# Kernel tuning notes

Measured on AMD Instinct MI355X. Metric: run time of the kernel, lower is better.

The kernel has to match this reference:

```python
import jax, jax.numpy as jnp
import numpy as np

N = 100000
E = 1600000
IN_C = 64
HID = 32
HEADS = 4
OUT_C = 1
NEG_SLOPE = 0.2
BN_EPS = 1e-5


def setup_inputs() -> dict:
    key = jax.random.key(0)
    ks = jax.random.split(key, 12)
    x = jax.random.normal(ks[0], (N, IN_C), dtype=jnp.float32)
    edge_index = jax.random.randint(ks[1], (2, E), 0, N, dtype=jnp.int32)
    # GATConv layer 1: in -> heads*hid, concat=True
    W1 = jax.random.normal(ks[2], (IN_C, HEADS * HID), dtype=jnp.float32) * (1.0 / np.sqrt(IN_C))
    att_src1 = jax.random.normal(ks[3], (HEADS, HID), dtype=jnp.float32) * 0.1
    att_dst1 = jax.random.normal(ks[4], (HEADS, HID), dtype=jnp.float32) * 0.1
    b1 = jnp.zeros((HEADS * HID,), dtype=jnp.float32)
    # GATConv layer 2: heads*hid -> out, heads=1, concat=False
    W2 = jax.random.normal(ks[5], (HEADS * HID, OUT_C), dtype=jnp.float32) * (1.0 / np.sqrt(HEADS * HID))
    att_src2 = jax.random.normal(ks[6], (1, OUT_C), dtype=jnp.float32) * 0.1
    att_dst2 = jax.random.normal(ks[7], (1, OUT_C), dtype=jnp.float32) * 0.1
    b2 = jnp.zeros((OUT_C,), dtype=jnp.float32)
    # BatchNorm1d (eval mode, running stats)
    bn_gamma = jnp.ones((HEADS * HID,), dtype=jnp.float32)
    bn_beta = jnp.zeros((HEADS * HID,), dtype=jnp.float32)
    bn_mean = jnp.zeros((HEADS * HID,), dtype=jnp.float32)
    bn_var = jnp.ones((HEADS * HID,), dtype=jnp.float32)
    return {"x": x, "edge_index": edge_index, "W1": W1, "att_src1": att_src1,
            "att_dst1": att_dst1, "b1": b1, "W2": W2, "att_src2": att_src2,
            "att_dst2": att_dst2, "b2": b2, "bn_gamma": bn_gamma, "bn_beta": bn_beta,
            "bn_mean": bn_mean, "bn_var": bn_var}


def _gat_layer(x, src, dst, W, a_src, a_dst, heads, out_c, n):
    # linear transform, split heads: [N, heads, out_c]
    h = (x @ W).reshape(n, heads, out_c)
    # per-node attention terms: [N, heads]
    alpha_s = jnp.einsum('nhc,hc->nh', h, a_src)
    alpha_d = jnp.einsum('nhc,hc->nh', h, a_dst)
    # edge logits: [E, heads]
    e = jax.nn.leaky_relu(alpha_s[src] + alpha_d[dst], NEG_SLOPE)
    # segment softmax over edges sharing a destination node
    e_max = jax.ops.segment_max(e, dst, num_segments=n)
    e = jnp.exp(e - e_max[dst])
    denom = jax.ops.segment_sum(e, dst, num_segments=n)
    alpha = e / (denom[dst] + 1e-16)                 # [E, heads]
    msg = h[src] * alpha[:, :, None]                 # [E, heads, out_c]
    return jax.ops.segment_sum(msg, dst, num_segments=n)  # [N, heads, out_c]


def reference(x, edge_index, W1, att_src1, att_dst1, b1, W2, att_src2, att_dst2,
              b2, bn_gamma, bn_beta, bn_mean, bn_var):
    n = x.shape[0]
    loops = jnp.arange(n, dtype=edge_index.dtype)
    src = jnp.concatenate([edge_index[0], loops])    # PyG GATConv adds self-loops
    dst = jnp.concatenate([edge_index[1], loops])
    # layer 1: concat heads
    h = _gat_layer(x, src, dst, W1, att_src1, att_dst1, HEADS, HID, n)
    h = h.reshape(n, HEADS * HID) + b1
    # BatchNorm1d (eval) + ELU (dropout is identity in eval)
    h = (h - bn_mean) * jax.lax.rsqrt(bn_var + BN_EPS) * bn_gamma + bn_beta
    h = jax.nn.elu(h)
    # layer 2: single head, concat=False (mean over 1 head == squeeze)
    out = _gat_layer(h, src, dst, W2, att_src2, att_dst2, 1, OUT_C, n)
    return out.reshape(n, OUT_C) + b2
```

## Files before the change

### kernel.cpp

```cpp
#include <hip/hip_runtime.h>
#include <cstdint>
#include <cstddef>

#define NEG_SLOPE 0.2f
#define BN_EPS 1e-5f
#define BK_SHIFT 8
#define MAXBK 512
#define CHUNK 8192
#define CAP 8192

typedef _Float16 half4 __attribute__((ext_vector_type(4)));

__global__ void prep_kernel(const float* __restrict__ b1,
                            const float* __restrict__ bn_gamma,
                            const float* __restrict__ bn_beta,
                            const float* __restrict__ bn_mean,
                            const float* __restrict__ bn_var,
                            float* __restrict__ pre0,
                            float* __restrict__ pre1,
                            int* __restrict__ bucket_cursor) {
    int t = threadIdx.x;
    if (t < 128) {
        float sc = rsqrtf(bn_var[t] + BN_EPS) * bn_gamma[t];
        pre0[t] = sc;
        pre1[t] = (b1[t] - bn_mean[t]) * sc + bn_beta[t];
    }
    if (t < MAXBK) bucket_cursor[t] = 0;
}

__global__ void bin_kernel(const int* __restrict__ ei, int E, int N, int NBK,
                           int* __restrict__ bucket_cursor,
                           unsigned int* __restrict__ binned) {
    __shared__ int cnt[MAXBK];
    __shared__ int gstart[MAXBK];
    __shared__ int cur[MAXBK];
    int T = E + N;
    int tid = threadIdx.x;
    for (int b = tid; b < NBK; b += 256) { cnt[b] = 0; cur[b] = 0; }
    __syncthreads();
    int base = blockIdx.x * CHUNK;
    bool fast = (base + CHUNK <= E);
    if (fast) {
        for (int k = 0; k < CHUNK; k += 1024) {
            int i0 = base + k + tid;
            int d0 = ei[E + i0];
            int d1 = ei[E + i0 + 256];
            int d2 = ei[E + i0 + 512];
            int d3 = ei[E + i0 + 768];
            atomicAdd(&cnt[d0 >> BK_SHIFT], 1);
            atomicAdd(&cnt[d1 >> BK_SHIFT], 1);
            atomicAdd(&cnt[d2 >> BK_SHIFT], 1);
            atomicAdd(&cnt[d3 >> BK_SHIFT], 1);
        }
    } else {
        for (int k = 0; k < CHUNK; k += 256) {
            int i = base + k + tid;
            if (i < T) {
                int dst = (i < E) ? ei[E + i] : (i - E);
                atomicAdd(&cnt[dst >> BK_SHIFT], 1);
            }
        }
    }
    __syncthreads();
    for (int b = tid; b < NBK; b += 256) {
        int c = cnt[b];
        if (c) gstart[b] = atomicAdd(&bucket_cursor[b], c);
    }
    __syncthreads();
    if (fast) {
        for (int k = 0; k < CHUNK; k += 1024) {
            int i0 = base + k + tid;
            int s0 = ei[i0];
            int s1 = ei[i0 + 256];
            int s2 = ei[i0 + 512];
            int s3 = ei[i0 + 768];
            int d0 = ei[E + i0];
            int d1 = ei[E + i0 + 256];
            int d2 = ei[E + i0 + 512];
            int d3 = ei[E + i0 + 768];
            int b0 = d0 >> BK_SHIFT, b1 = d1 >> BK_SHIFT;
            int b2 = d2 >> BK_SHIFT, b3 = d3 >> BK_SHIFT;
            int p0 = gstart[b0] + atomicAdd(&cur[b0], 1);
            int p1 = gstart[b1] + atomicAdd(&cur[b1], 1);
            int p2 = gstart[b2] + atomicAdd(&cur[b2], 1);
            int p3 = gstart[b3] + atomicAdd(&cur[b3], 1);
            if (p0 < CAP) binned[(size_t)b0 * CAP + p0] =
                (unsigned int)s0 | ((unsigned int)(d0 & 255) << 24);
            if (p1 < CAP) binned[(size_t)b1 * CAP + p1] =
                (unsigned int)s1 | ((unsigned int)(d1 & 255) << 24);
            if (p2 < CAP) binned[(size_t)b2 * CAP + p2] =
                (unsigned int)s2 | ((unsigned int)(d2 & 255) << 24);
            if (p3 < CAP) binned[(size_t)b3 * CAP + p3] =
                (unsigned int)s3 | ((unsigned int)(d3 & 255) << 24);
        }
    } else {
        for (int k = 0; k < CHUNK; k += 256) {
            int i = base + k + tid;
            if (i < T) {
                int src, dst;
                if (i < E) { src = ei[i]; dst = ei[E + i]; }
                else       { src = i - E; dst = src; }
                int b = dst >> BK_SHIFT;
                int lp = gstart[b] + atomicAdd(&cur[b], 1);
                if (lp < CAP)
                    binned[(size_t)b * CAP + lp] =
                        (unsigned int)src | ((unsigned int)(dst & 255) << 24);
            }
        }
    }
}

__global__ void gemm_kernel(const float* __restrict__ x,
                            const float* __restrict__ W1,
                            const float* __restrict__ att_s,
                            const float* __restrict__ att_d,
                            _Float16* __restrict__ h0,
                            float* __restrict__ as1,
                            float* __restrict__ ad1,
                            int N) {
    __shared__ float xs[512];
    int tid = threadIdx.x;
    int n0b = blockIdx.x * 8;
    if (n0b >= N) return;
    {
        const float* __restrict__ xb = x + (size_t)n0b * 64;
        int lim = N - n0b; if (lim > 8) lim = 8;
        int nf = lim * 64;
        for (int i = tid; i < 512; i += 256)
            xs[i] = (i < nf) ? xb[i] : 0.f;
    }
    __syncthreads();
    int c = tid & 127;
    int pair = __builtin_amdgcn_readfirstlane(tid >> 7);
    int n0 = n0b + pair * 4;
    if (n0 >= N) return;
    float acc[4] = {0.f, 0.f, 0.f, 0.f};
    const float4* __restrict__ xq = (const float4*)&xs[pair * 256];
#pragma unroll 2
    for (int kk = 0; kk < 16; ++kk) {
        float4 x0 = xq[kk];
        float4 x1 = xq[16 + kk];
        float4 x2 = xq[32 + kk];
        float4 x3 = xq[48 + kk];
        const float* __restrict__ wp = &W1[kk * 4 * 128 + c];
        float w0 = wp[0];
        float w1 = wp[128];
        float w2 = wp[256];
        float w3 = wp[384];
        acc[0] = fmaf(x0.x, w0, acc[0]); acc[0] = fmaf(x0.y, w1, acc[0]);
        acc[0] = fmaf(x0.z, w2, acc[0]); acc[0] = fmaf(x0.w, w3, acc[0]);
        acc[1] = fmaf(x1.x, w0, acc[1]); acc[1] = fmaf(x1.y, w1, acc[1]);
        acc[1] = fmaf(x1.z, w2, acc[1]); acc[1] = fmaf(x1.w, w3, acc[1]);
        acc[2] = fmaf(x2.x, w0, acc[2]); acc[2] = fmaf(x2.y, w1, acc[2]);
        acc[2] = fmaf(x2.z, w2, acc[2]); acc[2] = fmaf(x2.w, w3, acc[2]);
        acc[3] = fmaf(x3.x, w0, acc[3]); acc[3] = fmaf(x3.y, w1, acc[3]);
        acc[3] = fmaf(x3.z, w2, acc[3]); acc[3] = fmaf(x3.w, w3, acc[3]);
    }
    float asc = att_s[c], adc = att_d[c];
    int head = c >> 5;
    int nn = N - n0; if (nn > 4) nn = 4;
#pragma unroll
    for (int i = 0; i < 4; ++i) {
        if (i >= nn) break;
        int n = n0 + i;
        h0[(size_t)n * 128 + c] = (_Float16)acc[i];
        float s = acc[i] * asc;
        float d = acc[i] * adc;
#pragma unroll
        for (int off = 16; off >= 1; off >>= 1) {
            s += __shfl_xor(s, off);
            d += __shfl_xor(d, off);
        }
        if ((threadIdx.x & 31) == 0) {
            as1[(size_t)n * 4 + head] = s;
            ad1[(size_t)n * 4 + head] = d;
        }
    }
}

__global__ void csr_kernel(const unsigned int* __restrict__ binned,
                           const int* __restrict__ bucket_cursor,
                           int N,
                           int* __restrict__ row_beg,
                           int* __restrict__ row_end,
                           int* __restrict__ csr_src) {
    __shared__ int cnt[256];
    __shared__ int cur[256];
    __shared__ int wsum[4];
    int b = blockIdx.x;
    int tid = threadIdx.x;
    int n0 = b << BK_SHIFT;
    int nr = N - n0; if (nr > 256) nr = 256;
    int tot = bucket_cursor[b];
    if (tot > CAP) tot = CAP;
    size_t base = (size_t)b * CAP;
    if (tid < 256) cnt[tid] = 0;
    __syncthreads();
    for (int j = tid; j < tot; j += 1024) {
        atomicAdd(&cnt[binned[base + j] >> 24], 1);
    }
    __syncthreads();
    int v = 0, incl = 0;
    int lane = tid & 63;
    int w = tid >> 6;
    if (tid < 256) {
        v = cnt[tid];
        incl = v;
#pragma unroll
        for (int off = 1; off < 64; off <<= 1) {
            int t = __shfl_up(incl, off);
            if (lane >= off) incl += t;
        }
        if (lane == 63) wsum[w] = incl;
    }
    __syncthreads();
    if (tid < 256) {
        int prefix = 0;
#pragma unroll
        for (int i = 0; i < 3; ++i)
            if (i < w) prefix += wsum[i];
        incl += prefix;
        int excl = incl - v;
        cur[tid] = excl;
        if (tid < nr) {
            row_beg[n0 + tid] = (int)base + excl;
            row_end[n0 + tid] = (int)base + incl;
        }
    }
    __syncthreads();
    for (int j = tid; j < tot; j += 1024) {
        unsigned int wv = binned[base + j];
        int pos = atomicAdd(&cur[wv >> 24], 1);
        csr_src[base + pos] = (int)(wv & 0xFFFFFFu);
    }
}

__global__ void gather1_kernel(const int* __restrict__ row_beg,
                               const int* __restrict__ row_end,
                               const int* __restrict__ csr_src,
                               const half4* __restrict__ h0,
                               const float* __restrict__ as1,
                               const float* __restrict__ ad1,
                               const float* __restrict__ pre0,
                               const float* __restrict__ pre1,
                               const float* __restrict__ W2,
                               float* __restrict__ h2, int N) {
    int n = blockIdx.x * 4 + (threadIdx.x >> 6);
    if (n >= N) return;
    int lane = threadIdx.x & 63;
    int sub  = lane & 31;
    int grp  = lane >> 5;
    int head = sub >> 3;
    float ad = ad1[((unsigned)n << 2) + head];
    int beg = row_beg[n];
    int end = row_end[n];
    float4 acc = make_float4(0.f, 0.f, 0.f, 0.f);
    float den = 0.f;
#pragma unroll 2
    for (int j = beg + grp; j < end; j += 2) {
        int src = csr_src[j];
        float as = as1[((unsigned)src << 2) + head];
        float lg = as + ad;
        float l = fmaf(NEG_SLOPE, fminf(lg, 0.f), fmaxf(lg, 0.f));
        float w = __expf(l);
        half4 hv = h0[((unsigned)src << 5) + sub];
        acc.x = fmaf(w, (float)hv.x, acc.x);
        acc.y = fmaf(w, (float)hv.y, acc.y);
        acc.z = fmaf(w, (float)hv.z, acc.z);
        acc.w = fmaf(w, (float)hv.w, acc.w);
        den += w;
    }
    acc.x += __shfl_xor(acc.x, 32);
    acc.y += __shfl_xor(acc.y, 32);
    acc.z += __shfl_xor(acc.z, 32);
    acc.w += __shfl_xor(acc.w, 32);
    den   += __shfl_xor(den, 32);
    float inv = 1.f / (den + 1e-16f);
    int c = sub * 4;
    float v0 = fmaf(acc.x * inv, pre0[c],     pre1[c]);
    float v1 = fmaf(acc.y * inv, pre0[c + 1], pre1[c + 1]);
    float v2 = fmaf(acc.z * inv, pre0[c + 2], pre1[c + 2]);
    float v3 = fmaf(acc.w * inv, pre0[c + 3], pre1[c + 3]);
    v0 = v0 > 0.f ? v0 : __expf(v0) - 1.f;
    v1 = v1 > 0.f ? v1 : __expf(v1) - 1.f;
    v2 = v2 > 0.f ? v2 : __expf(v2) - 1.f;
    v3 = v3 > 0.f ? v3 : __expf(v3) - 1.f;
    float t = v0 * W2[c] + v1 * W2[c + 1] + v2 * W2[c + 2] + v3 * W2[c + 3];
#pragma unroll
    for (int off = 16; off >= 1; off >>= 1) t += __shfl_xor(t, off);
    if (lane == 0) h2[n] = t;
}

__global__ void gather2_kernel(const int* __restrict__ row_beg,
                               const int* __restrict__ row_end,
                               const int* __restrict__ csr_src,
                               const float* __restrict__ h2,
                               const float* __restrict__ att_s2,
                               const float* __restrict__ att_d2,
                               const float* __restrict__ b2,
                               float* __restrict__ out, int N) {
    int n = blockIdx.x * 16 + (threadIdx.x >> 4);
    if (n >= N) return;
    int lane = threadIdx.x & 15;
    int beg = row_beg[n];
    int end = row_end[n];
    float a_s = att_s2[0];
    float a_d = att_d2[0];
    float hd = h2[n];
    float num = 0.f, den = 0.f;
    for (int j = beg + lane; j < end; j += 16) {
        int src = csr_src[j];
        float hs = h2[src];
        float lg = hs * a_s + hd * a_d;
        float l = fmaf(NEG_SLOPE, fminf(lg, 0.f), fmaxf(lg, 0.f));
        float w = __expf(l);
        num += w * hs;
        den += w;
    }
#pragma unroll
    for (int off = 8; off >= 1; off >>= 1) {
        num += __shfl_xor(num, off);
        den += __shfl_xor(den, off);
    }
    if (lane == 0) out[n] = num / (den + 1e-16f) + b2[0];
}

extern "C" void kernel_launch(void* const* d_in, const int* in_sizes, int n_in,
                              void* d_out, int out_size, void* d_ws, size_t ws_size,
                              hipStream_t stream) {
    const float* x     = (const float*)d_in[0];
    const int*   ei    = (const int*)  d_in[1];
    const float* W1    = (const float*)d_in[2];
    const float* atts1 = (const float*)d_in[3];
    const float* attd1 = (const float*)d_in[4];
    const float* b1    = (const float*)d_in[5];
    const float* W2    = (const float*)d_in[6];
    const float* atts2 = (const float*)d_in[7];
    const float* attd2 = (const float*)d_in[8];
    const float* b2    = (const float*)d_in[9];
    const float* bn_g  = (const float*)d_in[10];
    const float* bn_b  = (const float*)d_in[11];
    const float* bn_m  = (const float*)d_in[12];
    const float* bn_v  = (const float*)d_in[13];

    const int N = in_sizes[0] / 64;
    const int E = in_sizes[1] / 2;
    const int T = E + N;
    const int NBK = (N + 255) >> BK_SHIFT;
    const int NCH = (T + CHUNK - 1) / CHUNK;
    const int NGB = (N + 7) / 8;

    char* p = (char*)d_ws;
    auto alloc = [&](size_t bytes, size_t align) -> void* {
        uintptr_t q = ((uintptr_t)p + align - 1) & ~(uintptr_t)(align - 1);
        p = (char*)(q + bytes);
        return (void*)q;
    };
    _Float16* h0      = (_Float16*)alloc((size_t)N * 128 * 2, 16);
    float* as1        = (float*)alloc((size_t)N * 4 * 4, 16);
    float* ad1        = (float*)alloc((size_t)N * 4 * 4, 16);
    float* h2         = (float*)alloc((size_t)N * 4, 16);
    float* pre0       = (float*)alloc(128 * 4, 16);
    float* pre1       = (float*)alloc(128 * 4, 16);
    int*   row_beg    = (int*)alloc((size_t)N * 4, 16);
    int*   row_end    = (int*)alloc((size_t)N * 4, 16);
    int*   bucket_cur = (int*)alloc((size_t)MAXBK * 4, 16);
    unsigned int* binned = (unsigned int*)alloc((size_t)NBK * CAP * 4, 16);
    int*   csr_src    = (int*)alloc((size_t)NBK * CAP * 4, 16);

    prep_kernel<<<1, 512, 0, stream>>>(b1, bn_g, bn_b, bn_m, bn_v,
                                       pre0, pre1, bucket_cur);

    bin_kernel<<<NCH, 256, 0, stream>>>(ei, E, N, NBK, bucket_cur, binned);

    gemm_kernel<<<NGB, 256, 0, stream>>>(x, W1, atts1, attd1, h0, as1, ad1, N);

    csr_kernel<<<NBK, 1024, 0, stream>>>(binned, bucket_cur, N,
                                         row_beg, row_end, csr_src);

    gather1_kernel<<<(N + 3) / 4, 256, 0, stream>>>(
        row_beg, row_end, csr_src, (const half4*)h0, as1, ad1, pre0, pre1,
        W2, h2, N);

    gather2_kernel<<<(N + 15) / 16, 256, 0, stream>>>(
        row_beg, row_end, csr_src, h2, atts2, attd2, b2, (float*)d_out, N);
}
```

Measured before the change: 268.8 us.

## Merge bin and GEMM kernels into one launch; compute two columns per lane

The edge-binning kernel and the layer-1 GEMM kernel are combined into one launch, with the first NCH blocks doing binning and the rest doing the GEMM. This removes a launch and lets the two independent stages overlap on the device. The GEMM part is also restructured so each lane computes two adjacent output columns for 16 nodes per block, using paired weight loads and half2 stores. This cuts the number of GEMM blocks and the shuffle depth. In exchange, every block reserves the larger shared-memory footprint of both paths, which may reduce occupancy.

After: 261.2 us. -2.8%, faster.

```diff
diff --git a/kernel.cpp b/kernel.cpp
--- a/kernel.cpp
+++ b/kernel.cpp
@@ -10,6 +10,14 @@
 #define CAP 8192
 
 typedef _Float16 half4 __attribute__((ext_vector_type(4)));
+typedef _Float16 half2v __attribute__((ext_vector_type(2)));
+typedef float float2v __attribute__((ext_vector_type(2)));
+
+static __device__ __forceinline__ float2v fma2(float2v w, float s, float2v a) {
+    a.x = fmaf(s, w.x, a.x);
+    a.y = fmaf(s, w.y, a.y);
+    return a;
+}
 
 __global__ void prep_kernel(const float* __restrict__ b1,
                             const float* __restrict__ bn_gamma,
@@ -28,154 +36,165 @@
     if (t < MAXBK) bucket_cursor[t] = 0;
 }
 
-__global__ void bin_kernel(const int* __restrict__ ei, int E, int N, int NBK,
-                           int* __restrict__ bucket_cursor,
-                           unsigned int* __restrict__ binned) {
+__global__ void gemm_bin_kernel(
+                                const float* __restrict__ x,
+                                const float* __restrict__ W1,
+                                const float* __restrict__ att_s,
+                                const float* __restrict__ att_d,
+                                _Float16* __restrict__ h0,
+                                float* __restrict__ as1,
+                                float* __restrict__ ad1,
+                                int N,
+                                const int* __restrict__ ei, int E, int NBK,
+                                int* __restrict__ bucket_cursor,
+                                unsigned int* __restrict__ binned,
+                                int NCH) {
     __shared__ int cnt[MAXBK];
     __shared__ int gstart[MAXBK];
     __shared__ int cur[MAXBK];
-    int T = E + N;
-    int tid = threadIdx.x;
-    for (int b = tid; b < NBK; b += 256) { cnt[b] = 0; cur[b] = 0; }
-    __syncthreads();
-    int base = blockIdx.x * CHUNK;
-    bool fast = (base + CHUNK <= E);
-    if (fast) {
-        for (int k = 0; k < CHUNK; k += 1024) {
-            int i0 = base + k + tid;
-            int d0 = ei[E + i0];
-            int d1 = ei[E + i0 + 256];
-            int d2 = ei[E + i0 + 512];
-            int d3 = ei[E + i0 + 768];
-            atomicAdd(&cnt[d0 >> BK_SHIFT], 1);
-            atomicAdd(&cnt[d1 >> BK_SHIFT], 1);
-            atomicAdd(&cnt[d2 >> BK_SHIFT], 1);
-            atomicAdd(&cnt[d3 >> BK_SHIFT], 1);
-        }
-    } else {
-        for (int k = 0; k < CHUNK; k += 256) {
-            int i = base + k + tid;
-            if (i < T) {
-                int dst = (i < E) ? ei[E + i] : (i - E);
-                atomicAdd(&cnt[dst >> BK_SHIFT], 1);
+    __shared__ float xs[1024];
+    if (blockIdx.x < NCH) {
+        int T = E + N;
+        int tid = threadIdx.x;
+        for (int b = tid; b < NBK; b += 256) { cnt[b] = 0; cur[b] = 0; }
+        __syncthreads();
+        int base = blockIdx.x * CHUNK;
+        bool fast = (base + CHUNK <= E);
+        if (fast) {
+            for (int k = 0; k < CHUNK; k += 1024) {
+                int i0 = base + k + tid;
+                int d0 = ei[E + i0];
+                int d1 = ei[E + i0 + 256];
+                int d2 = ei[E + i0 + 512];
+                int d3 = ei[E + i0 + 768];
+                atomicAdd(&cnt[d0 >> BK_SHIFT], 1);
+                atomicAdd(&cnt[d1 >> BK_SHIFT], 1);
+                atomicAdd(&cnt[d2 >> BK_SHIFT], 1);
+                atomicAdd(&cnt[d3 >> BK_SHIFT], 1);
+            }
+        } else {
+            for (int k = 0; k < CHUNK; k += 256) {
+                int i = base + k + tid;
+                if (i < T) {
+                    int dst = (i < E) ? ei[E + i] : (i - E);
+                    atomicAdd(&cnt[dst >> BK_SHIFT], 1);
+                }
             }
         }
-    }
-    __syncthreads();
-    for (int b = tid; b < NBK; b += 256) {
-        int c = cnt[b];
-        if (c) gstart[b] = atomicAdd(&bucket_cursor[b], c);
-    }
-    __syncthreads();
-    if (fast) {
-        for (int k = 0; k < CHUNK; k += 1024) {
-            int i0 = base + k + tid;
-            int s0 = ei[i0];
-            int s1 = ei[i0 + 256];
-            int s2 = ei[i0 + 512];
-            int s3 = ei[i0 + 768];
-            int d0 = ei[E + i0];
-            int d1 = ei[E + i0 + 256];
-            int d2 = ei[E + i0 + 512];
-            int d3 = ei[E + i0 + 768];
-            int b0 = d0 >> BK_SHIFT, b1 = d1 >> BK_SHIFT;
-            int b2 = d2 >> BK_SHIFT, b3 = d3 >> BK_SHIFT;
-            int p0 = gstart[b0] + atomicAdd(&cur[b0], 1);
-            int p1 = gstart[b1] + atomicAdd(&cur[b1], 1);
-            int p2 = gstart[b2] + atomicAdd(&cur[b2], 1);
-            int p3 = gstart[b3] + atomicAdd(&cur[b3], 1);
-            if (p0 < CAP) binned[(size_t)b0 * CAP + p0] =
-                (unsigned int)s0 | ((unsigned int)(d0 & 255) << 24);
-            if (p1 < CAP) binned[(size_t)b1 * CAP + p1] =
-                (unsigned int)s1 | ((unsigned int)(d1 & 255) << 24);
-            if (p2 < CAP) binned[(size_t)b2 * CAP + p2] =
-                (unsigned int)s2 | ((unsigned int)(d2 & 255) << 24);
-            if (p3 < CAP) binned[(size_t)b3 * CAP + p3] =
-                (unsigned int)s3 | ((unsigned int)(d3 & 255) << 24);
+        __syncthreads();
+        for (int b = tid; b < NBK; b += 256) {
+            int c = cnt[b];
+            if (c) gstart[b] = atomicAdd(&bucket_cursor[b], c);
         }
-    } else {
-        for (int k = 0; k < CHUNK; k += 256) {
-            int i = base + k + tid;
-            if (i < T) {
-                int src, dst;
-                if (i < E) { src = ei[i]; dst = ei[E + i]; }
-                else       { src = i - E; dst = src; }
-                int b = dst >> BK_SHIFT;
-                int lp = gstart[b] + atomicAdd(&cur[b], 1);
-                if (lp < CAP)
-                    binned[(size_t)b * CAP + lp] =
-                        (unsigned int)src | ((unsigned int)(dst & 255) << 24);
+        __syncthreads();
+        if (fast) {
+            for (int k = 0; k < CHUNK; k += 1024) {
+                int i0 = base + k + tid;
+                int s0 = ei[i0];
+                int s1 = ei[i0 + 256];
+                int s2 = ei[i0 + 512];
+                int s3 = ei[i0 + 768];
+                int d0 = ei[E + i0];
+                int d1 = ei[E + i0 + 256];
+                int d2 = ei[E + i0 + 512];
+                int d3 = ei[E + i0 + 768];
+                int b0 = d0 >> BK_SHIFT, b1 = d1 >> BK_SHIFT;
+                int b2 = d2 >> BK_SHIFT, b3 = d3 >> BK_SHIFT;
+                int p0 = gstart[b0] + atomicAdd(&cur[b0], 1);
+                int p1 = gstart[b1] + atomicAdd(&cur[b1], 1);
+                int p2 = gstart[b2] + atomicAdd(&cur[b2], 1);
+                int p3 = gstart[b3] + atomicAdd(&cur[b3], 1);
+                if (p0 < CAP) binned[(size_t)b0 * CAP + p0] =
+                    (unsigned int)s0 | ((unsigned int)(d0 & 255) << 24);
+                if (p1 < CAP) binned[(size_t)b1 * CAP + p1] =
+                    (unsigned int)s1 | ((unsigned int)(d1 & 255) << 24);
+                if (p2 < CAP) binned[(size_t)b2 * CAP + p2] =
+                    (unsigned int)s2 | ((unsigned int)(d2 & 255) << 24);
+                if (p3 < CAP) binned[(size_t)b3 * CAP + p3] =
+                    (unsigned int)s3 | ((unsigned int)(d3 & 255) << 24);
+            }
+        } else {
+            for (int k = 0; k < CHUNK; k += 256) {
+                int i = base + k + tid;
+                if (i < T) {
+                    int src, dst;
+                    if (i < E) { src = ei[i]; dst = ei[E + i]; }
+                    else       { src = i - E; dst = src; }
+                    int b = dst >> BK_SHIFT;
+                    int lp = gstart[b] + atomicAdd(&cur[b], 1);
+                    if (lp < CAP)
+                        binned[(size_t)b * CAP + lp] =
+                            (unsigned int)src | ((unsigned int)(dst & 255) << 24);
+                }
             }
         }
-    }
-}
-
-__global__ void gemm_kernel(const float* __restrict__ x,
-                            const float* __restrict__ W1,
-                            const float* __restrict__ att_s,
-                            const float* __restrict__ att_d,
-                            _Float16* __restrict__ h0,
-                            float* __restrict__ as1,
-                            float* __restrict__ ad1,
-                            int N) {
-    __shared__ float xs[512];
+        return;
+    }
+    int bid = blockIdx.x - NCH;
     int tid = threadIdx.x;
-    int n0b = blockIdx.x * 8;
+    int n0b = bid * 16;
     if (n0b >= N) return;
     {
         const float* __restrict__ xb = x + (size_t)n0b * 64;
-        int lim = N - n0b; if (lim > 8) lim = 8;
+        int lim = N - n0b; if (lim > 16) lim = 16;
         int nf = lim * 64;
-        for (int i = tid; i < 512; i += 256)
+        for (int i = tid; i < 1024; i += 256)
             xs[i] = (i < nf) ? xb[i] : 0.f;
     }
     __syncthreads();
-    int c = tid & 127;
-    int pair = __builtin_amdgcn_readfirstlane(tid >> 7);
-    int n0 = n0b + pair * 4;
+    int lane = tid & 63;
+    int c2 = lane * 2;
+    int wv = __builtin_amdgcn_readfirstlane(tid >> 6);
+    int n0 = n0b + wv * 4;
     if (n0 >= N) return;
-    float acc[4] = {0.f, 0.f, 0.f, 0.f};
-    const float4* __restrict__ xq = (const float4*)&xs[pair * 256];
+    float2v acc0 = {0.f, 0.f}, acc1 = {0.f, 0.f};
+    float2v acc2 = {0.f, 0.f}, acc3 = {0.f, 0.f};
+    const float4* __restrict__ xq = (const float4*)&xs[wv * 256];
 #pragma unroll 2
     for (int kk = 0; kk < 16; ++kk) {
         float4 x0 = xq[kk];
         float4 x1 = xq[16 + kk];
         float4 x2 = xq[32 + kk];
         float4 x3 = xq[48 + kk];
-        const float* __restrict__ wp = &W1[kk * 4 * 128 + c];
-        float w0 = wp[0];
-        float w1 = wp[128];
-        float w2 = wp[256];
-        float w3 = wp[384];
-        acc[0] = fmaf(x0.x, w0, acc[0]); acc[0] = fmaf(x0.y, w1, acc[0]);
-        acc[0] = fmaf(x0.z, w2, acc[0]); acc[0] = fmaf(x0.w, w3, acc[0]);
-        acc[1] = fmaf(x1.x, w0, acc[1]); acc[1] = fmaf(x1.y, w1, acc[1]);
-        acc[1] = fmaf(x1.z, w2, acc[1]); acc[1] = fmaf(x1.w, w3, acc[1]);
-        acc[2] = fmaf(x2.x, w0, acc[2]); acc[2] = fmaf(x2.y, w1, acc[2]);
-        acc[2] = fmaf(x2.z, w2, acc[2]); acc[2] = fmaf(x2.w, w3, acc[2]);
-        acc[3] = fmaf(x3.x, w0, acc[3]); acc[3] = fmaf(x3.y, w1, acc[3]);
-        acc[3] = fmaf(x3.z, w2, acc[3]); acc[3] = fmaf(x3.w, w3, acc[3]);
-    }
-    float asc = att_s[c], adc = att_d[c];
-    int head = c >> 5;
-    int nn = N - n0; if (nn > 4) nn = 4;
-#pragma unroll
-    for (int i = 0; i < 4; ++i) {
-        if (i >= nn) break;
-        int n = n0 + i;
-        h0[(size_t)n * 128 + c] = (_Float16)acc[i];
-        float s = acc[i] * asc;
-        float d = acc[i] * adc;
-#pragma unroll
-        for (int off = 16; off >= 1; off >>= 1) {
-            s += __shfl_xor(s, off);
-            d += __shfl_xor(d, off);
-        }
-        if ((threadIdx.x & 31) == 0) {
-            as1[(size_t)n * 4 + head] = s;
-            ad1[(size_t)n * 4 + head] = d;
-        }
-    }
+        float2v w0 = *(const float2v*)&W1[(kk * 4 + 0) * 128 + c2];
+        float2v w1 = *(const float2v*)&W1[(kk * 4 + 1) * 128 + c2];
+        float2v w2 = *(const float2v*)&W1[(kk * 4 + 2) * 128 + c2];
+        float2v w3 = *(const float2v*)&W1[(kk * 4 + 3) * 128 + c2];
+        acc0 = fma2(w0, x0.x, acc0); acc0 = fma2(w1, x0.y, acc0);
+        acc0 = fma2(w2, x0.z, acc0); acc0 = fma2(w3, x0.w, acc0);
+        acc1 = fma2(w0, x1.x, acc1); acc1 = fma2(w1, x1.y, acc1);
+        acc1 = fma2(w2, x1.z, acc1); acc1 = fma2(w3, x1.w, acc1);
+        acc2 = fma2(w0, x2.x, acc2); acc2 = fma2(w1, x2.y, acc2);
+        acc2 = fma2(w2, x2.z, acc2); acc2 = fma2(w3, x2.w, acc2);
+        acc3 = fma2(w0, x3.x, acc3); acc3 = fma2(w1, x3.y, acc3);
+        acc3 = fma2(w2, x3.z, acc3); acc3 = fma2(w3, x3.w, acc3);
+    }
+    float asA = att_s[c2], asB = att_s[c2 + 1];
+    float adA = att_d[c2], adB = att_d[c2 + 1];
+    int head = lane >> 4;
+#define GEMM_EPI(ACC, I)                                                      \
+    {                                                                         \
+        int n = n0 + (I);                                                     \
+        if (n < N) {                                                          \
+            half2v hv; hv.x = (_Float16)(ACC).x; hv.y = (_Float16)(ACC).y;    \
+            *(half2v*)&h0[(size_t)n * 128 + c2] = hv;                         \
+            float s = (ACC).x * asA + (ACC).y * asB;                          \
+            float d = (ACC).x * adA + (ACC).y * adB;                          \
+            s += __shfl_xor(s, 8); d += __shfl_xor(d, 8);                     \
+            s += __shfl_xor(s, 4); d += __shfl_xor(d, 4);                     \
+            s += __shfl_xor(s, 2); d += __shfl_xor(d, 2);                     \
+            s += __shfl_xor(s, 1); d += __shfl_xor(d, 1);                     \
+            if ((lane & 15) == 0) {                                           \
+                as1[(size_t)n * 4 + head] = s;                                \
+                ad1[(size_t)n * 4 + head] = d;                                \
+            }                                                                 \
+        }                                                                     \
+    }
+    GEMM_EPI(acc0, 0)
+    GEMM_EPI(acc1, 1)
+    GEMM_EPI(acc2, 2)
+    GEMM_EPI(acc3, 3)
+#undef GEMM_EPI
 }
 
 __global__ void csr_kernel(const unsigned int* __restrict__ binned,
@@ -348,7 +367,7 @@
     const int T = E + N;
     const int NBK = (N + 255) >> BK_SHIFT;
     const int NCH = (T + CHUNK - 1) / CHUNK;
-    const int NGB = (N + 7) / 8;
+    const int NGB = (N + 15) / 16;
 
     char* p = (char*)d_ws;
     auto alloc = [&](size_t bytes, size_t align) -> void* {
@@ -371,9 +390,9 @@
     prep_kernel<<<1, 512, 0, stream>>>(b1, bn_g, bn_b, bn_m, bn_v,
                                        pre0, pre1, bucket_cur);
 
-    bin_kernel<<<NCH, 256, 0, stream>>>(ei, E, N, NBK, bucket_cur, binned);
-
-    gemm_kernel<<<NGB, 256, 0, stream>>>(x, W1, atts1, attd1, h0, as1, ad1, N);
+    gemm_bin_kernel<<<NCH + NGB, 256, 0, stream>>>(
+        x, W1, atts1, attd1, h0, as1, ad1, N,
+        ei, E, NBK, bucket_cur, binned, NCH);
 
     csr_kernel<<<NBK, 1024, 0, stream>>>(binned, bucket_cur, N,
                                          row_beg, row_end, csr_src);
```

## Build CSR via global degree count, scans, and direct atomic scatter fused with GEMM

Applied to the files above, without the earlier changes.

Replaces the bucketed binning plus per-bucket CSR kernel with a global per-node degree histogram, a two-level prefix scan, and a direct scatter of source indices using per-node global atomics. The scatter is merged into the GEMM launch as extra blocks so the two independent jobs can run concurrently. This removes the intermediate binned buffer and its fixed-capacity padding, and the CSR becomes compact. In exchange it adds about 3.2M global atomics to random addresses (degree counting and cursor increments) plus scattered 4-byte writes, which may contend and cost more than the shared-memory atomics they replace.

Result: slower. 377.2 us (+40.3%).

```diff
diff --git a/kernel.cpp b/kernel.cpp
--- a/kernel.cpp
+++ b/kernel.cpp
@@ -5,9 +5,8 @@
 #define NEG_SLOPE 0.2f
 #define BN_EPS 1e-5f
 #define BK_SHIFT 8
-#define MAXBK 512
 #define CHUNK 8192
-#define CAP 8192
+#define DCHUNK 4096
 
 typedef _Float16 half4 __attribute__((ext_vector_type(4)));
 
@@ -17,46 +16,46 @@
                             const float* __restrict__ bn_mean,
                             const float* __restrict__ bn_var,
                             float* __restrict__ pre0,
-                            float* __restrict__ pre1,
-                            int* __restrict__ bucket_cursor) {
+                            float* __restrict__ pre1) {
     int t = threadIdx.x;
     if (t < 128) {
         float sc = rsqrtf(bn_var[t] + BN_EPS) * bn_gamma[t];
         pre0[t] = sc;
         pre1[t] = (b1[t] - bn_mean[t]) * sc + bn_beta[t];
     }
-    if (t < MAXBK) bucket_cursor[t] = 0;
-}
-
-__global__ void bin_kernel(const int* __restrict__ ei, int E, int N, int NBK,
-                           int* __restrict__ bucket_cursor,
-                           unsigned int* __restrict__ binned) {
-    __shared__ int cnt[MAXBK];
-    __shared__ int gstart[MAXBK];
-    __shared__ int cur[MAXBK];
+}
+
+__global__ void deg_kernel(const int* __restrict__ ei, int E, int N, int NBK,
+                           int* __restrict__ deg, int* __restrict__ bktsum) {
+    __shared__ int cnt[512];
     int T = E + N;
     int tid = threadIdx.x;
-    for (int b = tid; b < NBK; b += 256) { cnt[b] = 0; cur[b] = 0; }
+    for (int b = tid; b < NBK; b += 256) cnt[b] = 0;
     __syncthreads();
-    int base = blockIdx.x * CHUNK;
-    bool fast = (base + CHUNK <= E);
+    int base = blockIdx.x * DCHUNK;
+    bool fast = (base + DCHUNK <= E);
     if (fast) {
-        for (int k = 0; k < CHUNK; k += 1024) {
+        for (int k = 0; k < DCHUNK; k += 1024) {
             int i0 = base + k + tid;
             int d0 = ei[E + i0];
             int d1 = ei[E + i0 + 256];
             int d2 = ei[E + i0 + 512];
             int d3 = ei[E + i0 + 768];
+            atomicAdd(&deg[d0], 1);
+            atomicAdd(&deg[d1], 1);
+            atomicAdd(&deg[d2], 1);
+            atomicAdd(&deg[d3], 1);
             atomicAdd(&cnt[d0 >> BK_SHIFT], 1);
             atomicAdd(&cnt[d1 >> BK_SHIFT], 1);
             atomicAdd(&cnt[d2 >> BK_SHIFT], 1);
             atomicAdd(&cnt[d3 >> BK_SHIFT], 1);
         }
     } else {
-        for (int k = 0; k < CHUNK; k += 256) {
+        for (int k = 0; k < DCHUNK; k += 256) {
             int i = base + k + tid;
             if (i < T) {
                 int dst = (i < E) ? ei[E + i] : (i - E);
+                atomicAdd(&deg[dst], 1);
                 atomicAdd(&cnt[dst >> BK_SHIFT], 1);
             }
         }
@@ -64,63 +63,124 @@
     __syncthreads();
     for (int b = tid; b < NBK; b += 256) {
         int c = cnt[b];
-        if (c) gstart[b] = atomicAdd(&bucket_cursor[b], c);
-    }
+        if (c) atomicAdd(&bktsum[b], c);
+    }
+}
+
+__global__ void scan_bkt_kernel(const int* __restrict__ bktsum, int NBK,
+                                int* __restrict__ bucket_base) {
+    int lane = threadIdx.x;
+    int cpl = (NBK + 63) >> 6;
+    int beg = lane * cpl;
+    int s = 0;
+    for (int i = 0; i < cpl; ++i) {
+        int b = beg + i;
+        if (b < NBK) s += bktsum[b];
+    }
+    int incl = s;
+#pragma unroll
+    for (int off = 1; off < 64; off <<= 1) {
+        int t = __shfl_up(incl, off);
+        if (lane >= off) incl += t;
+    }
+    int run = incl - s;
+    for (int i = 0; i < cpl; ++i) {
+        int b = beg + i;
+        if (b < NBK) { bucket_base[b] = run; run += bktsum[b]; }
+    }
+}
+
+__global__ void scan_row_kernel(const int* __restrict__ deg,
+                                const int* __restrict__ bucket_base,
+                                int N,
+                                int* __restrict__ row_beg,
+                                int* __restrict__ row_end,
+                                int* __restrict__ cur) {
+    __shared__ int wsum[4];
+    int b = blockIdx.x;
+    int tid = threadIdx.x;
+    int n = (b << BK_SHIFT) + tid;
+    int v = (n < N) ? deg[n] : 0;
+    int lane = tid & 63;
+    int w = tid >> 6;
+    int incl = v;
+#pragma unroll
+    for (int off = 1; off < 64; off <<= 1) {
+        int t = __shfl_up(incl, off);
+        if (lane >= off) incl += t;
+    }
+    if (lane == 63) wsum[w] = incl;
     __syncthreads();
-    if (fast) {
-        for (int k = 0; k < CHUNK; k += 1024) {
-            int i0 = base + k + tid;
-            int s0 = ei[i0];
-            int s1 = ei[i0 + 256];
-            int s2 = ei[i0 + 512];
-            int s3 = ei[i0 + 768];
-            int d0 = ei[E + i0];
-            int d1 = ei[E + i0 + 256];
-            int d2 = ei[E + i0 + 512];
-            int d3 = ei[E + i0 + 768];
-            int b0 = d0 >> BK_SHIFT, b1 = d1 >> BK_SHIFT;
-            int b2 = d2 >> BK_SHIFT, b3 = d3 >> BK_SHIFT;
-            int p0 = gstart[b0] + atomicAdd(&cur[b0], 1);
-            int p1 = gstart[b1] + atomicAdd(&cur[b1], 1);
-            int p2 = gstart[b2] + atomicAdd(&cur[b2], 1);
-            int p3 = gstart[b3] + atomicAdd(&cur[b3], 1);
-            if (p0 < CAP) binned[(size_t)b0 * CAP + p0] =
-                (unsigned int)s0 | ((unsigned int)(d0 & 255) << 24);
-            if (p1 < CAP) binned[(size_t)b1 * CAP + p1] =
-                (unsigned int)s1 | ((unsigned int)(d1 & 255) << 24);
-            if (p2 < CAP) binned[(size_t)b2 * CAP + p2] =
-                (unsigned int)s2 | ((unsigned int)(d2 & 255) << 24);
-            if (p3 < CAP) binned[(size_t)b3 * CAP + p3] =
-                (unsigned int)s3 | ((unsigned int)(d3 & 255) << 24);
-        }
-    } else {
-        for (int k = 0; k < CHUNK; k += 256) {
-            int i = base + k + tid;
-            if (i < T) {
-                int src, dst;
-                if (i < E) { src = ei[i]; dst = ei[E + i]; }
-                else       { src = i - E; dst = src; }
-                int b = dst >> BK_SHIFT;
-                int lp = gstart[b] + atomicAdd(&cur[b], 1);
-                if (lp < CAP)
-                    binned[(size_t)b * CAP + lp] =
-                        (unsigned int)src | ((unsigned int)(dst & 255) << 24);
+    int prefix = 0;
+#pragma unroll
+    for (int i = 0; i < 3; ++i)
+        if (i < w) prefix += wsum[i];
+    incl += prefix;
+    int base = bucket_base[b];
+    if (n < N) {
+        int excl = incl - v;
+        row_beg[n] = base + excl;
+        row_end[n] = base + incl;
+        cur[n]     = base + excl;
+    }
+}
+
+__global__ void scatter_gemm_kernel(
+                                    const float* __restrict__ x,
+                                    const float* __restrict__ W1,
+                                    const float* __restrict__ att_s,
+                                    const float* __restrict__ att_d,
+                                    _Float16* __restrict__ h0,
+                                    float* __restrict__ as1,
+                                    float* __restrict__ ad1,
+                                    int N,
+                                    const int* __restrict__ ei, int E,
+                                    int* __restrict__ cur,
+                                    int* __restrict__ csr_src,
+                                    int NSC) {
+    __shared__ float xs[512];
+    if (blockIdx.x < NSC) {
+        int T = E + N;
+        int tid = threadIdx.x;
+        int base = blockIdx.x * CHUNK;
+        bool fast = (base + CHUNK <= E);
+        if (fast) {
+            for (int k = 0; k < CHUNK; k += 1024) {
+                int i0 = base + k + tid;
+                int s0 = ei[i0];
+                int s1 = ei[i0 + 256];
+                int s2 = ei[i0 + 512];
+                int s3 = ei[i0 + 768];
+                int d0 = ei[E + i0];
+                int d1 = ei[E + i0 + 256];
+                int d2 = ei[E + i0 + 512];
+                int d3 = ei[E + i0 + 768];
+                int p0 = atomicAdd(&cur[d0], 1);
+                int p1 = atomicAdd(&cur[d1], 1);
+                int p2 = atomicAdd(&cur[d2], 1);
+                int p3 = atomicAdd(&cur[d3], 1);
+                csr_src[p0] = s0;
+                csr_src[p1] = s1;
+                csr_src[p2] = s2;
+                csr_src[p3] = s3;
             }
-        }
-    }
-}
-
-__global__ void gemm_kernel(const float* __restrict__ x,
-                            const float* __restrict__ W1,
-                            const float* __restrict__ att_s,
-                            const float* __restrict__ att_d,
-                            _Float16* __restrict__ h0,
-                            float* __restrict__ as1,
-                            float* __restrict__ ad1,
-                            int N) {
-    __shared__ float xs[512];
+        } else {
+            for (int k = 0; k < CHUNK; k += 256) {
+                int i = base + k + tid;
+                if (i < T) {
+                    int src, dst;
+                    if (i < E) { src = ei[i]; dst = ei[E + i]; }
+                    else       { src = i - E; dst = src; }
+                    int p = atomicAdd(&cur[dst], 1);
+                    csr_src[p] = src;
+                }
+            }
+        }
+        return;
+    }
+    int bid = blockIdx.x - NSC;
     int tid = threadIdx.x;
-    int n0b = blockIdx.x * 8;
+    int n0b = bid * 8;
     if (n0b >= N) return;
     {
         const float* __restrict__ xb = x + (size_t)n0b * 64;
@@ -175,63 +235,6 @@
             as1[(size_t)n * 4 + head] = s;
             ad1[(size_t)n * 4 + head] = d;
         }
-    }
-}
-
-__global__ void csr_kernel(const unsigned int* __restrict__ binned,
-                           const int* __restrict__ bucket_cursor,
-                           int N,
-                           int* __restrict__ row_beg,
-                           int* __restrict__ row_end,
-                           int* __restrict__ csr_src) {
-    __shared__ int cnt[256];
-    __shared__ int cur[256];
-    __shared__ int wsum[4];
-    int b = blockIdx.x;
-    int tid = threadIdx.x;
-    int n0 = b << BK_SHIFT;
-    int nr = N - n0; if (nr > 256) nr = 256;
-    int tot = bucket_cursor[b];
-    if (tot > CAP) tot = CAP;
-    size_t base = (size_t)b * CAP;
-    if (tid < 256) cnt[tid] = 0;
-    __syncthreads();
-    for (int j = tid; j < tot; j += 1024) {
-        atomicAdd(&cnt[binned[base + j] >> 24], 1);
-    }
-    __syncthreads();
-    int v = 0, incl = 0;
-    int lane = tid & 63;
-    int w = tid >> 6;
-    if (tid < 256) {
-        v = cnt[tid];
-        incl = v;
-#pragma unroll
-        for (int off = 1; off < 64; off <<= 1) {
-            int t = __shfl_up(incl, off);
-            if (lane >= off) incl += t;
-        }
-        if (lane == 63) wsum[w] = incl;
-    }
-    __syncthreads();
-    if (tid < 256) {
-        int prefix = 0;
-#pragma unroll
-        for (int i = 0; i < 3; ++i)
-            if (i < w) prefix += wsum[i];
-        incl += prefix;
-        int excl = incl - v;
-        cur[tid] = excl;
-        if (tid < nr) {
-            row_beg[n0 + tid] = (int)base + excl;
-            row_end[n0 + tid] = (int)base + incl;
-        }
-    }
-    __syncthreads();
-    for (int j = tid; j < tot; j += 1024) {
-        unsigned int wv = binned[base + j];
-        int pos = atomicAdd(&cur[wv >> 24], 1);
-        csr_src[base + pos] = (int)(wv & 0xFFFFFFu);
     }
 }
 
@@ -347,7 +350,8 @@
     const int E = in_sizes[1] / 2;
     const int T = E + N;
     const int NBK = (N + 255) >> BK_SHIFT;
-    const int NCH = (T + CHUNK - 1) / CHUNK;
+    const int NDG = (T + DCHUNK - 1) / DCHUNK;
+    const int NSC = (T + CHUNK - 1) / CHUNK;
     const int NGB = (N + 7) / 8;
 
     char* p = (char*)d_ws;
@@ -364,19 +368,26 @@
     float* pre1       = (float*)alloc(128 * 4, 16);
     int*   row_beg    = (int*)alloc((size_t)N * 4, 16);
     int*   row_end    = (int*)alloc((size_t)N * 4, 16);
-    int*   bucket_cur = (int*)alloc((size_t)MAXBK * 4, 16);
-    unsigned int* binned = (unsigned int*)alloc((size_t)NBK * CAP * 4, 16);
-    int*   csr_src    = (int*)alloc((size_t)NBK * CAP * 4, 16);
-
-    prep_kernel<<<1, 512, 0, stream>>>(b1, bn_g, bn_b, bn_m, bn_v,
-                                       pre0, pre1, bucket_cur);
-
-    bin_kernel<<<NCH, 256, 0, stream>>>(ei, E, N, NBK, bucket_cur, binned);
-
-    gemm_kernel<<<NGB, 256, 0, stream>>>(x, W1, atts1, attd1, h0, as1, ad1, N);
-
-    csr_kernel<<<NBK, 1024, 0, stream>>>(binned, bucket_cur, N,
-                                         row_beg, row_end, csr_src);
+    int*   deg        = (int*)alloc(((size_t)N + 512) * 4, 16);
+    int*   bktsum     = deg + N;
+    int*   bucket_base= (int*)alloc(512 * 4, 16);
+    int*   cur        = (int*)alloc((size_t)N * 4, 16);
+    int*   csr_src    = (int*)alloc((size_t)T * 4, 16);
+
+    hipMemsetAsync(deg, 0, ((size_t)N + 512) * 4, stream);
+
+    prep_kernel<<<1, 128, 0, stream>>>(b1, bn_g, bn_b, bn_m, bn_v, pre0, pre1);
+
+    deg_kernel<<<NDG, 256, 0, stream>>>(ei, E, N, NBK, deg, bktsum);
+
+    scan_bkt_kernel<<<1, 64, 0, stream>>>(bktsum, NBK, bucket_base);
+
+    scan_row_kernel<<<NBK, 256, 0, stream>>>(deg, bucket_base, N,
+                                             row_beg, row_end, cur);
+
+    scatter_gemm_kernel<<<NSC + NGB, 256, 0, stream>>>(
+        x, W1, atts1, attd1, h0, as1, ad1, N,
+        ei, E, cur, csr_src, NSC);
 
     gather1_kernel<<<(N + 3) / 4, 256, 0, stream>>>(
         row_beg, row_end, csr_src, (const half4*)h0, as1, ad1, pre0, pre1,
```

## Fuse CSR build and node GEMM into one heterogeneous kernel launch

Applied to the files above, without the earlier changes.

Merges the CSR construction kernel and the dense feature GEMM kernel into a single launch. The first NBK blocks build per-bucket CSR rows, and the remaining blocks run the GEMM with 1024 threads covering 32 nodes each. The two independent workloads can then overlap on the GPU, and one launch and its serialization gap go away. In exchange the GEMM blocks now carry the CSR path's shared memory and larger block size, which may lower occupancy.

Measured after the change: 267.8 us. No clear change (-0.4%).

```diff
diff --git a/kernel.cpp b/kernel.cpp
--- a/kernel.cpp
+++ b/kernel.cpp
@@ -110,32 +110,95 @@
     }
 }
 
-__global__ void gemm_kernel(const float* __restrict__ x,
-                            const float* __restrict__ W1,
-                            const float* __restrict__ att_s,
-                            const float* __restrict__ att_d,
-                            _Float16* __restrict__ h0,
-                            float* __restrict__ as1,
-                            float* __restrict__ ad1,
-                            int N) {
-    __shared__ float xs[512];
+__global__ void csr_gemm_kernel(
+                                const unsigned int* __restrict__ binned,
+                                const int* __restrict__ bucket_cursor,
+                                int* __restrict__ row_beg,
+                                int* __restrict__ row_end,
+                                int* __restrict__ csr_src,
+                                int NBK, int N,
+                                const float* __restrict__ x,
+                                const float* __restrict__ W1,
+                                const float* __restrict__ att_s,
+                                const float* __restrict__ att_d,
+                                _Float16* __restrict__ h0,
+                                float* __restrict__ as1,
+                                float* __restrict__ ad1) {
+    __shared__ int cnt[256];
+    __shared__ int cur[256];
+    __shared__ int wsum[4];
+    __shared__ float xs[2048];
+    if ((int)blockIdx.x < NBK) {
+        int b = blockIdx.x;
+        int tid = threadIdx.x;
+        int n0 = b << BK_SHIFT;
+        int nr = N - n0; if (nr > 256) nr = 256;
+        int tot = bucket_cursor[b];
+        if (tot > CAP) tot = CAP;
+        size_t base = (size_t)b * CAP;
+        if (tid < 256) cnt[tid] = 0;
+        __syncthreads();
+        for (int j = tid; j < tot; j += 1024) {
+            atomicAdd(&cnt[binned[base + j] >> 24], 1);
+        }
+        __syncthreads();
+        int v = 0, incl = 0;
+        int lane = tid & 63;
+        int w = tid >> 6;
+        if (tid < 256) {
+            v = cnt[tid];
+            incl = v;
+#pragma unroll
+            for (int off = 1; off < 64; off <<= 1) {
+                int t = __shfl_up(incl, off);
+                if (lane >= off) incl += t;
+            }
+            if (lane == 63) wsum[w] = incl;
+        }
+        __syncthreads();
+        if (tid < 256) {
+            int prefix = 0;
+#pragma unroll
+            for (int i = 0; i < 3; ++i)
+                if (i < w) prefix += wsum[i];
+            incl += prefix;
+            int excl = incl - v;
+            cur[tid] = excl;
+            if (tid < nr) {
+                row_beg[n0 + tid] = (int)base + excl;
+                row_end[n0 + tid] = (int)base + incl;
+            }
+        }
+        __syncthreads();
+        for (int j = tid; j < tot; j += 1024) {
+            unsigned int wv = binned[base + j];
+            int pos = atomicAdd(&cur[wv >> 24], 1);
+            csr_src[base + pos] = (int)(wv & 0xFFFFFFu);
+        }
+        return;
+    }
+    int bid = blockIdx.x - NBK;
     int tid = threadIdx.x;
-    int n0b = blockIdx.x * 8;
-    if (n0b >= N) return;
-    {
+    int q    = __builtin_amdgcn_readfirstlane(tid >> 8);
+    int t    = tid & 255;
+    int n0b  = bid * 32 + q * 8;
+    bool qvalid = (n0b < N);
+    if (qvalid) {
         const float* __restrict__ xb = x + (size_t)n0b * 64;
         int lim = N - n0b; if (lim > 8) lim = 8;
         int nf = lim * 64;
-        for (int i = tid; i < 512; i += 256)
-            xs[i] = (i < nf) ? xb[i] : 0.f;
+        float* __restrict__ xq_s = &xs[q * 512];
+        for (int i = t; i < 512; i += 256)
+            xq_s[i] = (i < nf) ? xb[i] : 0.f;
     }
     __syncthreads();
-    int c = tid & 127;
-    int pair = __builtin_amdgcn_readfirstlane(tid >> 7);
+    if (!qvalid) return;
+    int c = t & 127;
+    int pair = __builtin_amdgcn_readfirstlane((t >> 7) & 1);
     int n0 = n0b + pair * 4;
     if (n0 >= N) return;
     float acc[4] = {0.f, 0.f, 0.f, 0.f};
-    const float4* __restrict__ xq = (const float4*)&xs[pair * 256];
+    const float4* __restrict__ xq = (const float4*)&xs[q * 512 + pair * 256];
 #pragma unroll 2
     for (int kk = 0; kk < 16; ++kk) {
         float4 x0 = xq[kk];
@@ -171,67 +234,10 @@
             s += __shfl_xor(s, off);
             d += __shfl_xor(d, off);
         }
-        if ((threadIdx.x & 31) == 0) {
+        if ((t & 31) == 0) {
             as1[(size_t)n * 4 + head] = s;
             ad1[(size_t)n * 4 + head] = d;
         }
-    }
-}
-
-__global__ void csr_kernel(const unsigned int* __restrict__ binned,
-                           const int* __restrict__ bucket_cursor,
-                           int N,
-                           int* __restrict__ row_beg,
-                           int* __restrict__ row_end,
-                           int* __restrict__ csr_src) {
-    __shared__ int cnt[256];
-    __shared__ int cur[256];
-    __shared__ int wsum[4];
-    int b = blockIdx.x;
-    int tid = threadIdx.x;
-    int n0 = b << BK_SHIFT;
-    int nr = N - n0; if (nr > 256) nr = 256;
-    int tot = bucket_cursor[b];
-    if (tot > CAP) tot = CAP;
-    size_t base = (size_t)b * CAP;
-    if (tid < 256) cnt[tid] = 0;
-    __syncthreads();
-    for (int j = tid; j < tot; j += 1024) {
-        atomicAdd(&cnt[binned[base + j] >> 24], 1);
-    }
-    __syncthreads();
-    int v = 0, incl = 0;
-    int lane = tid & 63;
-    int w = tid >> 6;
-    if (tid < 256) {
-        v = cnt[tid];
-        incl = v;
-#pragma unroll
-        for (int off = 1; off < 64; off <<= 1) {
-            int t = __shfl_up(incl, off);
-            if (lane >= off) incl += t;
-        }
-        if (lane == 63) wsum[w] = incl;
-    }
-    __syncthreads();
-    if (tid < 256) {
-        int prefix = 0;
-#pragma unroll
-        for (int i = 0; i < 3; ++i)
-            if (i < w) prefix += wsum[i];
-        incl += prefix;
-        int excl = incl - v;
-        cur[tid] = excl;
-        if (tid < nr) {
-            row_beg[n0 + tid] = (int)base + excl;
-            row_end[n0 + tid] = (int)base + incl;
-        }
-    }
-    __syncthreads();
-    for (int j = tid; j < tot; j += 1024) {
-        unsigned int wv = binned[base + j];
-        int pos = atomicAdd(&cur[wv >> 24], 1);
-        csr_src[base + pos] = (int)(wv & 0xFFFFFFu);
     }
 }
 
@@ -348,7 +354,7 @@
     const int T = E + N;
     const int NBK = (N + 255) >> BK_SHIFT;
     const int NCH = (T + CHUNK - 1) / CHUNK;
-    const int NGB = (N + 7) / 8;
+    const int NGB = (N + 31) / 32;
 
     char* p = (char*)d_ws;
     auto alloc = [&](size_t bytes, size_t align) -> void* {
@@ -373,10 +379,9 @@
 
     bin_kernel<<<NCH, 256, 0, stream>>>(ei, E, N, NBK, bucket_cur, binned);
 
-    gemm_kernel<<<NGB, 256, 0, stream>>>(x, W1, atts1, attd1, h0, as1, ad1, N);
-
-    csr_kernel<<<NBK, 1024, 0, stream>>>(binned, bucket_cur, N,
-                                         row_beg, row_end, csr_src);
+    csr_gemm_kernel<<<NBK + NGB, 1024, 0, stream>>>(
+        binned, bucket_cur, row_beg, row_end, csr_src, NBK, N,
+        x, W1, atts1, attd1, h0, as1, ad1);
 
     gather1_kernel<<<(N + 3) / 4, 256, 0, stream>>>(
         row_beg, row_end, csr_src, (const half4*)h0, as1, ad1, pre0, pre1,
```
